# Kernel optimization log

Hardware: AMD Instinct MI355X
Metric: run time of the kernel (lower is better)

Reference implementation:

```python
import jax, jax.numpy as jnp
import numpy as np

NUM_ANCHORS = 5
NUM_CLASSES = 20


def setup_inputs() -> dict:
    key = jax.random.key(0)
    k1, k2, k3, k4 = jax.random.split(key, 4)
    N, H, W, M = 64, 52, 52, 32
    img = 1664
    x = jax.random.normal(k1, (N, NUM_ANCHORS * (5 + NUM_CLASSES), H, W), jnp.float32)
    anchors = jnp.array([[1.08, 1.19], [3.42, 4.41], [6.63, 11.38],
                         [9.42, 5.11], [16.62, 10.52]], jnp.float32)
    # valid gt boxes in xyxy pixel coords
    xy = jax.random.uniform(k2, (N, M, 2), jnp.float32) * (img * 0.8)
    wh = jax.random.uniform(k3, (N, M, 2), jnp.float32) * (img * 0.2) + 1.0
    gt_boxes = jnp.concatenate([xy, xy + wh], axis=-1)
    gt_labels = jax.random.randint(k4, (N, M), 0, NUM_CLASSES)
    return dict(x=x, anchors=anchors, gt_boxes=gt_boxes, gt_labels=gt_labels,
                img_h=img, img_w=img)


def _format_outputs(x, anchors, img_h, img_w):
    # x: [N, A*(5+C), H, W] -> (coords [N,HW,A,4] (x,y,w,h), obj [N,HW,A], scores [N,HW,A,C])
    N, _, H, W = x.shape
    A = anchors.shape[0]
    t = x.reshape(N, A, 5 + NUM_CLASSES, H, W).transpose(0, 3, 4, 1, 2)  # [N,H,W,A,5+C]
    c_x = jnp.arange(W, dtype=x.dtype) * (img_w / W)
    c_y = jnp.arange(H, dtype=x.dtype) * (img_h / H)
    b_x = jax.nn.sigmoid(t[..., 0]) + c_x[None, None, :, None]   # [N,H,W,A]
    b_y = jax.nn.sigmoid(t[..., 1]) + c_y[None, :, None, None]
    b_w = (img_w / W) * anchors[:, 0] * jnp.exp(t[..., 2])
    b_h = (img_h / H) * anchors[:, 1] * jnp.exp(t[..., 3])
    coords = jnp.stack([b_x, b_y, b_w, b_h], axis=-1).reshape(N, H * W, A, 4)
    b_o = jax.nn.sigmoid(t[..., 4]).reshape(N, H * W, A)
    scores = t[..., 5:].reshape(N, H * W, A, NUM_CLASSES)
    return coords, b_o, scores


def reference(x, anchors, gt_boxes, gt_labels, img_h, img_w):
    coords, b_o, scores = _format_outputs(x, anchors, img_h, img_w)
    # pred_boxes[..., 2:] += pred_boxes[..., :2]  (xywh -> xyxy)
    boxes = jnp.concatenate([coords[..., :2], coords[..., :2] + coords[..., 2:]], axis=-1)  # [N,HW,A,4]
    # box_iou: pred [N,HW,A,1,4] vs gt [N,1,1,M,4] -> [N,HW,A,M]
    p = boxes[..., None, :]
    g = gt_boxes[:, None, None, :, :]
    lt = jnp.maximum(p[..., :2], g[..., :2])
    rb = jnp.minimum(p[..., 2:], g[..., 2:])
    whi = jnp.clip(rb - lt, 0.0)
    inter = whi[..., 0] * whi[..., 1]
    area_p = (boxes[..., 2] - boxes[..., 0]) * (boxes[..., 3] - boxes[..., 1])
    area_g = (gt_boxes[..., 2] - gt_boxes[..., 0]) * (gt_boxes[..., 3] - gt_boxes[..., 1])
    iou = inter / (area_p[..., None] + area_g[:, None, None, :] - inter)   # [N,HW,A,M]

    cell_sel = iou.max(axis=(2, 3)) > 0.0                 # [N,HW]
    best_a = jnp.argmax(iou.max(axis=3), axis=2)          # [N,HW] best anchor per cell
    iou_best = jnp.take_along_axis(iou, best_a[..., None, None], axis=2)[:, :, 0, :]  # [N,HW,M]
    max_iou = iou_best.max(axis=-1)                       # [N,HW]
    gt_idx = jnp.argmax(iou_best, axis=-1)                # [N,HW]

    sel_box = jnp.take_along_axis(boxes, best_a[..., None, None], axis=2)[:, :, 0, :]   # [N,HW,4]
    sel_o = jnp.take_along_axis(b_o, best_a[..., None], axis=2)[:, :, 0]                # [N,HW]
    sel_sc = jnp.take_along_axis(scores, best_a[..., None, None], axis=2)[:, :, 0, :]   # [N,HW,C]
    g_box = jnp.take_along_axis(gt_boxes, gt_idx[..., None], axis=1)                    # [N,HW,4]
    g_lab = jnp.take_along_axis(gt_labels, gt_idx, axis=1)                              # [N,HW]

    m = cell_sel.astype(x.dtype)
    objectness_loss = (jnp.sum(m * (sel_o - max_iou) ** 2)
                       + 0.5 * jnp.sum((1.0 - m) * b_o.max(axis=2) ** 2))
    bbox_loss = (jnp.sum(m * jnp.sum((sel_box[..., :2] - g_box[..., :2]) ** 2, axis=-1))
                 + jnp.sum(m * jnp.sum((jnp.sqrt(sel_box[..., 2:]) - jnp.sqrt(g_box[..., 2:])) ** 2, axis=-1)))
    logp = jax.nn.log_softmax(sel_sc, axis=-1)
    ce = -jnp.take_along_axis(logp, g_lab[..., None], axis=-1)[..., 0]
    clf_loss = jnp.sum(m * ce)
    return jnp.stack([objectness_loss, bbox_loss, clf_loss])
```

## Files before the change

### kernel.cpp

```cpp
#include <hip/hip_runtime.h>
#include <math.h>

#define A_ 5
#define C_ 20
#define N_ 64
#define H_ 52
#define W_ 52
#define HW_ (H_ * W_)
#define M_ 32
#define CH_ (A_ * (5 + C_))
#define CPB 64
#define NBLK_X ((HW_ + CPB - 1) / CPB)
#define NBLK (NBLK_X * N_)

__global__ __launch_bounds__(320) void yolo_main(
    const float* __restrict__ x,
    const float* __restrict__ anchors,
    const float* __restrict__ gt,
    const int* __restrict__ glab,
    const void* img_h_p, const void* img_w_p,
    float* __restrict__ ws)
{
    __shared__ float s_c[8][A_][CPB];

    const int tid  = threadIdx.x;
    const int a    = tid >> 6;
    const int lane = tid & 63;
    const int n    = blockIdx.y;
    const int cell = blockIdx.x * CPB + lane;
    const bool valid = cell < HW_;

    int ibw = *(const int*)img_w_p;
    float img_w = (ibw > 0 && ibw < 1000000) ? (float)ibw : *(const float*)img_w_p;
    int ibh = *(const int*)img_h_p;
    float img_h = (ibh > 0 && ibh < 1000000) ? (float)ibh : *(const float*)img_h_p;
    const float sx = img_w / (float)W_;
    const float sy = img_h / (float)H_;

    const float ax = anchors[2 * a];
    const float ay = anchors[2 * a + 1];

    float bi = 0.f, bu = 1.f;
    int   bm = 0;
    float x1 = 0.f, y1 = 0.f, x2 = 0.f, y2 = 0.f, ov = 0.f;

    if (valid) {
        const int wi = cell % W_;
        const int hi = cell / W_;
        const size_t base = (size_t)n * CH_ * HW_ + (size_t)a * 25 * HW_ + cell;
        float t0 = x[base];
        float t1 = x[base + (size_t)HW_];
        float t2 = x[base + 2 * (size_t)HW_];
        float t3 = x[base + 3 * (size_t)HW_];
        float t4 = x[base + 4 * (size_t)HW_];

        float bx = 1.f / (1.f + __expf(-t0)) + (float)wi * sx;
        float by = 1.f / (1.f + __expf(-t1)) + (float)hi * sy;
        float bw = sx * ax * __expf(t2);
        float bh = sy * ay * __expf(t3);
        x1 = bx; y1 = by; x2 = bx + bw; y2 = by + bh;
        ov = 1.f / (1.f + __expf(-t4));
        float ap = (x2 - x1) * (y2 - y1);

        const float4* gtv = (const float4*)(gt + (size_t)n * M_ * 4);
        #pragma unroll 8
        for (int m = 0; m < M_; ++m) {
            float4 g = gtv[m];
            float area = (g.z - g.x) * (g.w - g.y);
            float wxi = fminf(x2, g.z) - fmaxf(x1, g.x);
            float hyi = fminf(y2, g.w) - fmaxf(y1, g.y);
            wxi = fmaxf(wxi, 0.f);
            hyi = fmaxf(hyi, 0.f);
            float inter = wxi * hyi;
            float uni = ap + area - inter;
            if (inter * bu > bi * uni) { bi = inter; bu = uni; bm = m; }
        }
    }

    s_c[0][a][lane] = bi;
    s_c[1][a][lane] = bu;
    s_c[2][a][lane] = x1;
    s_c[3][a][lane] = y1;
    s_c[4][a][lane] = x2;
    s_c[5][a][lane] = y2;
    s_c[6][a][lane] = ov;
    s_c[7][a][lane] = __int_as_float(bm);
    __syncthreads();

    if (tid < 64) {
        float obj = 0.f, bbx = 0.f, clf = 0.f;

        float Bi = 0.f, Bu = 1.f;
        int Ba = 0, Bm = 0;
        float X1 = 0.f, Y1 = 0.f, X2 = 0.f, Y2 = 0.f, O = 0.f;
        float bomax = -1e30f;
        #pragma unroll
        for (int aa = 0; aa < A_; ++aa) {
            float ci = s_c[0][aa][lane];
            float cu = s_c[1][aa][lane];
            float co = s_c[6][aa][lane];
            bomax = fmaxf(bomax, co);
            bool upd = (aa == 0) || (ci * Bu > Bi * cu);
            if (upd) {
                Bi = ci; Bu = cu; Ba = aa;
                Bm = __float_as_int(s_c[7][aa][lane]);
                X1 = s_c[2][aa][lane]; Y1 = s_c[3][aa][lane];
                X2 = s_c[4][aa][lane]; Y2 = s_c[5][aa][lane];
                O = co;
            }
        }

        if (valid) {
            if (Bi > 0.f) {
                float miou = Bi / Bu;
                float d = O - miou;
                obj = d * d;

                float4 g = ((const float4*)gt)[n * M_ + Bm];
                float d0 = X1 - g.x;
                float d1 = Y1 - g.y;
                float d2 = sqrtf(X2) - sqrtf(g.z);
                float d3 = sqrtf(Y2) - sqrtf(g.w);
                bbx = d0 * d0 + d1 * d1 + d2 * d2 + d3 * d3;

                const size_t sb = (size_t)n * CH_ * HW_ + (size_t)(Ba * 25 + 5) * HW_ + cell;
                const int lab = glab[n * M_ + Bm];
                float mx = -1e30f, se = 0.f, scl = 0.f;
                #pragma unroll
                for (int j = 0; j < C_; ++j) {
                    float v = x[sb + (size_t)j * HW_];
                    float nm = fmaxf(mx, v);
                    se = se * __expf(mx - nm) + __expf(v - nm);
                    mx = nm;
                    scl = (j == lab) ? v : scl;
                }
                clf = mx + __logf(se) - scl;
            } else {
                obj = 0.5f * bomax * bomax;
            }
        }

        #pragma unroll
        for (int off = 32; off > 0; off >>= 1) {
            obj += __shfl_down(obj, off, 64);
            bbx += __shfl_down(bbx, off, 64);
            clf += __shfl_down(clf, off, 64);
        }
        if (tid == 0) {
            const int bid = blockIdx.y * gridDim.x + blockIdx.x;
            ws[bid * 3 + 0] = obj;
            ws[bid * 3 + 1] = bbx;
            ws[bid * 3 + 2] = clf;
        }
    }
}

__global__ __launch_bounds__(256) void yolo_reduce(
    const float* __restrict__ ws, float* __restrict__ out)
{
    __shared__ float s_red[4][3];
    const int tid = threadIdx.x;
    float o = 0.f, b = 0.f, c = 0.f;
    for (int e = tid; e < NBLK; e += 256) {
        o += ws[e * 3 + 0];
        b += ws[e * 3 + 1];
        c += ws[e * 3 + 2];
    }
    #pragma unroll
    for (int off = 32; off > 0; off >>= 1) {
        o += __shfl_down(o, off, 64);
        b += __shfl_down(b, off, 64);
        c += __shfl_down(c, off, 64);
    }
    const int wid = tid >> 6;
    if ((tid & 63) == 0) {
        s_red[wid][0] = o; s_red[wid][1] = b; s_red[wid][2] = c;
    }
    __syncthreads();
    if (tid == 0) {
        float oo = 0.f, bb = 0.f, cc = 0.f;
        #pragma unroll
        for (int w = 0; w < 4; ++w) {
            oo += s_red[w][0]; bb += s_red[w][1]; cc += s_red[w][2];
        }
        out[0] = oo; out[1] = bb; out[2] = cc;
    }
}

extern "C" void kernel_launch(void* const* d_in, const int* in_sizes, int n_in,
                              void* d_out, int out_size, void* d_ws, size_t ws_size,
                              hipStream_t stream) {
    const float* x    = (const float*)d_in[0];
    const float* anch = (const float*)d_in[1];
    const float* gt   = (const float*)d_in[2];
    const int*   gl   = (const int*)d_in[3];
    const void*  ih   = d_in[4];
    const void*  iw   = d_in[5];
    float* out = (float*)d_out;
    float* ws  = (float*)d_ws;

    dim3 grid(NBLK_X, N_);
    yolo_main<<<grid, dim3(320), 0, stream>>>(x, anch, gt, gl, ih, iw, ws);
    yolo_reduce<<<1, 256, 0, stream>>>(ws, out);
}
```

Baseline: 142.6 us.

## Process two cells per thread with float2 loads and spread epilogue across two waves

Each thread now handles two adjacent cells, loading its five anchor channels as float2 and reusing each ground-truth box load for both cells in the IoU loop. The per-cell epilogue (anchor selection, softmax cross-entropy) now runs on 128 threads instead of 64, and partial sums go through a shared-memory cross-wave reduction. This halves the block count and the redundant GT reads, but raises register pressure and relies on HW_ being even for float2 alignment.

```diff
diff --git a/kernel.cpp b/kernel.cpp
--- a/kernel.cpp
+++ b/kernel.cpp
@@ -9,9 +9,9 @@
 #define HW_ (H_ * W_)
 #define M_ 32
 #define CH_ (A_ * (5 + C_))
-#define CPB 64
-#define NBLK_X ((HW_ + CPB - 1) / CPB)
-#define NBLK (NBLK_X * N_)
+#define CPB 128
+#define NBX ((HW_ + CPB - 1) / CPB)
+#define NBLK (NBX * N_)
 
 __global__ __launch_bounds__(320) void yolo_main(
     const float* __restrict__ x,
@@ -22,13 +22,14 @@
     float* __restrict__ ws)
 {
     __shared__ float s_c[8][A_][CPB];
+    __shared__ float s_red[5][3];
 
     const int tid  = threadIdx.x;
     const int a    = tid >> 6;
     const int lane = tid & 63;
     const int n    = blockIdx.y;
-    const int cell = blockIdx.x * CPB + lane;
-    const bool valid = cell < HW_;
+    const int c0   = blockIdx.x * CPB + 2 * lane;
+    const bool v2  = c0 < HW_;
 
     int ibw = *(const int*)img_w_p;
     float img_w = (ibw > 0 && ibw < 1000000) ? (float)ibw : *(const float*)img_w_p;
@@ -40,118 +41,140 @@
     const float ax = anchors[2 * a];
     const float ay = anchors[2 * a + 1];
 
-    float bi = 0.f, bu = 1.f;
-    int   bm = 0;
-    float x1 = 0.f, y1 = 0.f, x2 = 0.f, y2 = 0.f, ov = 0.f;
-
-    if (valid) {
-        const int wi = cell % W_;
-        const int hi = cell / W_;
-        const size_t base = (size_t)n * CH_ * HW_ + (size_t)a * 25 * HW_ + cell;
-        float t0 = x[base];
-        float t1 = x[base + (size_t)HW_];
-        float t2 = x[base + 2 * (size_t)HW_];
-        float t3 = x[base + 3 * (size_t)HW_];
-        float t4 = x[base + 4 * (size_t)HW_];
-
-        float bx = 1.f / (1.f + __expf(-t0)) + (float)wi * sx;
-        float by = 1.f / (1.f + __expf(-t1)) + (float)hi * sy;
-        float bw = sx * ax * __expf(t2);
-        float bh = sy * ay * __expf(t3);
-        x1 = bx; y1 = by; x2 = bx + bw; y2 = by + bh;
-        ov = 1.f / (1.f + __expf(-t4));
-        float ap = (x2 - x1) * (y2 - y1);
-
-        const float4* gtv = (const float4*)(gt + (size_t)n * M_ * 4);
-        #pragma unroll 8
-        for (int m = 0; m < M_; ++m) {
-            float4 g = gtv[m];
-            float area = (g.z - g.x) * (g.w - g.y);
-            float wxi = fminf(x2, g.z) - fmaxf(x1, g.x);
-            float hyi = fminf(y2, g.w) - fmaxf(y1, g.y);
+    float X1[2] = {0.f, 0.f}, Y1[2] = {0.f, 0.f}, X2[2] = {0.f, 0.f}, Y2[2] = {0.f, 0.f};
+    float AP[2] = {0.f, 0.f}, OV[2] = {0.f, 0.f};
+    float bi[2] = {0.f, 0.f}, bu[2] = {1.f, 1.f};
+    int   bm[2] = {0, 0};
+
+    if (v2) {
+        const size_t base = (size_t)n * CH_ * HW_ + (size_t)a * 25 * HW_ + c0;
+        const float2* p = (const float2*)(x + base);
+        float2 t0 = p[0];
+        float2 t1 = p[HW_ / 2];
+        float2 t2 = p[HW_];
+        float2 t3 = p[3 * HW_ / 2];
+        float2 t4 = p[2 * HW_];
+        #pragma unroll
+        for (int s = 0; s < 2; ++s) {
+            const int cell = c0 + s;
+            const int wi = cell % W_;
+            const int hi = cell / W_;
+            float u0 = s ? t0.y : t0.x;
+            float u1 = s ? t1.y : t1.x;
+            float u2 = s ? t2.y : t2.x;
+            float u3 = s ? t3.y : t3.x;
+            float u4 = s ? t4.y : t4.x;
+            float bx = 1.f / (1.f + __expf(-u0)) + (float)wi * sx;
+            float by = 1.f / (1.f + __expf(-u1)) + (float)hi * sy;
+            float bw = sx * ax * __expf(u2);
+            float bh = sy * ay * __expf(u3);
+            X1[s] = bx; Y1[s] = by; X2[s] = bx + bw; Y2[s] = by + bh;
+            AP[s] = (X2[s] - X1[s]) * (Y2[s] - Y1[s]);
+            OV[s] = 1.f / (1.f + __expf(-u4));
+        }
+    }
+
+    const float4* gtv = (const float4*)(gt + (size_t)n * M_ * 4);
+    #pragma unroll 4
+    for (int m = 0; m < M_; ++m) {
+        float4 g = gtv[m];
+        float area = (g.z - g.x) * (g.w - g.y);
+        #pragma unroll
+        for (int s = 0; s < 2; ++s) {
+            float wxi = fminf(X2[s], g.z) - fmaxf(X1[s], g.x);
+            float hyi = fminf(Y2[s], g.w) - fmaxf(Y1[s], g.y);
             wxi = fmaxf(wxi, 0.f);
             hyi = fmaxf(hyi, 0.f);
             float inter = wxi * hyi;
-            float uni = ap + area - inter;
-            if (inter * bu > bi * uni) { bi = inter; bu = uni; bm = m; }
-        }
-    }
-
-    s_c[0][a][lane] = bi;
-    s_c[1][a][lane] = bu;
-    s_c[2][a][lane] = x1;
-    s_c[3][a][lane] = y1;
-    s_c[4][a][lane] = x2;
-    s_c[5][a][lane] = y2;
-    s_c[6][a][lane] = ov;
-    s_c[7][a][lane] = __int_as_float(bm);
+            float uni = AP[s] + area - inter;
+            if (inter * bu[s] > bi[s] * uni) { bi[s] = inter; bu[s] = uni; bm[s] = m; }
+        }
+    }
+
+    {
+        float2* pl;
+        pl = (float2*)&s_c[0][a][0]; pl[lane] = make_float2(bi[0], bi[1]);
+        pl = (float2*)&s_c[1][a][0]; pl[lane] = make_float2(bu[0], bu[1]);
+        pl = (float2*)&s_c[2][a][0]; pl[lane] = make_float2(__int_as_float(bm[0]), __int_as_float(bm[1]));
+        pl = (float2*)&s_c[3][a][0]; pl[lane] = make_float2(OV[0], OV[1]);
+        pl = (float2*)&s_c[4][a][0]; pl[lane] = make_float2(X1[0], X1[1]);
+        pl = (float2*)&s_c[5][a][0]; pl[lane] = make_float2(Y1[0], Y1[1]);
+        pl = (float2*)&s_c[6][a][0]; pl[lane] = make_float2(X2[0], X2[1]);
+        pl = (float2*)&s_c[7][a][0]; pl[lane] = make_float2(Y2[0], Y2[1]);
+    }
     __syncthreads();
 
-    if (tid < 64) {
-        float obj = 0.f, bbx = 0.f, clf = 0.f;
-
-        float Bi = 0.f, Bu = 1.f;
+    float obj = 0.f, bbx = 0.f, clf = 0.f;
+    const int tcell = blockIdx.x * CPB + tid;
+    if (tid < CPB && tcell < HW_) {
+        float Bi = 0.f, Bu = 1.f, O = 0.f;
+        float BX1 = 0.f, BY1 = 0.f, BX2 = 0.f, BY2 = 0.f;
         int Ba = 0, Bm = 0;
-        float X1 = 0.f, Y1 = 0.f, X2 = 0.f, Y2 = 0.f, O = 0.f;
         float bomax = -1e30f;
         #pragma unroll
         for (int aa = 0; aa < A_; ++aa) {
-            float ci = s_c[0][aa][lane];
-            float cu = s_c[1][aa][lane];
-            float co = s_c[6][aa][lane];
+            float ci = s_c[0][aa][tid];
+            float cu = s_c[1][aa][tid];
+            float co = s_c[3][aa][tid];
             bomax = fmaxf(bomax, co);
             bool upd = (aa == 0) || (ci * Bu > Bi * cu);
             if (upd) {
-                Bi = ci; Bu = cu; Ba = aa;
-                Bm = __float_as_int(s_c[7][aa][lane]);
-                X1 = s_c[2][aa][lane]; Y1 = s_c[3][aa][lane];
-                X2 = s_c[4][aa][lane]; Y2 = s_c[5][aa][lane];
-                O = co;
+                Bi = ci; Bu = cu; Ba = aa; O = co;
+                Bm = __float_as_int(s_c[2][aa][tid]);
+                BX1 = s_c[4][aa][tid]; BY1 = s_c[5][aa][tid];
+                BX2 = s_c[6][aa][tid]; BY2 = s_c[7][aa][tid];
             }
         }
 
-        if (valid) {
-            if (Bi > 0.f) {
-                float miou = Bi / Bu;
-                float d = O - miou;
-                obj = d * d;
-
-                float4 g = ((const float4*)gt)[n * M_ + Bm];
-                float d0 = X1 - g.x;
-                float d1 = Y1 - g.y;
-                float d2 = sqrtf(X2) - sqrtf(g.z);
-                float d3 = sqrtf(Y2) - sqrtf(g.w);
-                bbx = d0 * d0 + d1 * d1 + d2 * d2 + d3 * d3;
-
-                const size_t sb = (size_t)n * CH_ * HW_ + (size_t)(Ba * 25 + 5) * HW_ + cell;
-                const int lab = glab[n * M_ + Bm];
-                float mx = -1e30f, se = 0.f, scl = 0.f;
-                #pragma unroll
-                for (int j = 0; j < C_; ++j) {
-                    float v = x[sb + (size_t)j * HW_];
-                    float nm = fmaxf(mx, v);
-                    se = se * __expf(mx - nm) + __expf(v - nm);
-                    mx = nm;
-                    scl = (j == lab) ? v : scl;
-                }
-                clf = mx + __logf(se) - scl;
-            } else {
-                obj = 0.5f * bomax * bomax;
+        if (Bi > 0.f) {
+            float miou = Bi / Bu;
+            float d = O - miou;
+            obj = d * d;
+
+            float4 g = ((const float4*)gt)[n * M_ + Bm];
+            float d0 = BX1 - g.x;
+            float d1 = BY1 - g.y;
+            float d2 = sqrtf(BX2) - sqrtf(g.z);
+            float d3 = sqrtf(BY2) - sqrtf(g.w);
+            bbx = d0 * d0 + d1 * d1 + d2 * d2 + d3 * d3;
+
+            const size_t sb = (size_t)n * CH_ * HW_ + (size_t)(Ba * 25 + 5) * HW_ + tcell;
+            const int lab = glab[n * M_ + Bm];
+            float mx = -1e30f, se = 0.f, scl = 0.f;
+            #pragma unroll
+            for (int j = 0; j < C_; ++j) {
+                float v = x[sb + (size_t)j * HW_];
+                float nm = fmaxf(mx, v);
+                se = se * __expf(mx - nm) + __expf(v - nm);
+                mx = nm;
+                scl = (j == lab) ? v : scl;
             }
-        }
-
-        #pragma unroll
-        for (int off = 32; off > 0; off >>= 1) {
-            obj += __shfl_down(obj, off, 64);
-            bbx += __shfl_down(bbx, off, 64);
-            clf += __shfl_down(clf, off, 64);
-        }
-        if (tid == 0) {
-            const int bid = blockIdx.y * gridDim.x + blockIdx.x;
-            ws[bid * 3 + 0] = obj;
-            ws[bid * 3 + 1] = bbx;
-            ws[bid * 3 + 2] = clf;
-        }
+            clf = mx + __logf(se) - scl;
+        } else {
+            obj = 0.5f * bomax * bomax;
+        }
+    }
+
+    #pragma unroll
+    for (int off = 32; off > 0; off >>= 1) {
+        obj += __shfl_down(obj, off, 64);
+        bbx += __shfl_down(bbx, off, 64);
+        clf += __shfl_down(clf, off, 64);
+    }
+    if (lane == 0) {
+        s_red[a][0] = obj; s_red[a][1] = bbx; s_red[a][2] = clf;
+    }
+    __syncthreads();
+    if (tid == 0) {
+        float oo = 0.f, bb = 0.f, cc = 0.f;
+        #pragma unroll
+        for (int w = 0; w < 5; ++w) {
+            oo += s_red[w][0]; bb += s_red[w][1]; cc += s_red[w][2];
+        }
+        const int bid = blockIdx.y * gridDim.x + blockIdx.x;
+        ws[bid * 3 + 0] = oo;
+        ws[bid * 3 + 1] = bb;
+        ws[bid * 3 + 2] = cc;
     }
 }
 
@@ -199,7 +222,7 @@
     float* out = (float*)d_out;
     float* ws  = (float*)d_ws;
 
-    dim3 grid(NBLK_X, N_);
+    dim3 grid(NBX, N_);
     yolo_main<<<grid, dim3(320), 0, stream>>>(x, anch, gt, gl, ih, iw, ws);
     yolo_reduce<<<1, 256, 0, stream>>>(ws, out);
 }
```

After: 146.8 us. 3.0% more time.
